# Performance work log

Hardware: AMD Instinct MI355X
Metric: run time of the kernel (lower is better)

## Reference

```python
import jax, jax.numpy as jnp
import numpy as np

BN_EPS = 1e-3          # nn.BatchNorm1d(..., eps=0.001)
NUM_PILLARS = 600000   # M = total occupied pillars across the batch
N_POINTS = 3_000_000
C_IN, C_OUT = 10, 64


def setup_inputs() -> dict:
    key = jax.random.key(0)
    k1, k2, k3 = jax.random.split(key, 3)
    pts_feature = jax.random.normal(k1, (N_POINTS, C_IN), dtype=jnp.float32)
    point_pillar_indices = jax.random.randint(k2, (N_POINTS,), 0, NUM_PILLARS, dtype=jnp.int32)
    # Linear(C_IN, C_OUT, bias=False), kaiming_normal init
    W = jax.random.normal(k3, (C_IN, C_OUT), dtype=jnp.float32) * np.sqrt(2.0 / C_IN)
    # BatchNorm1d in eval mode (running stats)
    gamma = jnp.ones((C_OUT,), jnp.float32)
    beta = jnp.zeros((C_OUT,), jnp.float32)
    run_mean = jnp.zeros((C_OUT,), jnp.float32)
    run_var = jnp.ones((C_OUT,), jnp.float32)
    return {"pts_feature": pts_feature, "point_pillar_indices": point_pillar_indices,
            "W": W, "gamma": gamma, "beta": beta, "run_mean": run_mean, "run_var": run_var}


def reference(pts_feature, point_pillar_indices, W, gamma, beta, run_mean, run_var):
    # shared MLP: Linear(no bias) -> BatchNorm1d(eval) -> ReLU, fused per-point
    h = pts_feature @ W                                        # (N, C_OUT)
    h = gamma * (h - run_mean) * jax.lax.rsqrt(run_var + BN_EPS) + beta
    h = jax.nn.relu(h)
    # scatter_max over irregular pillar ids -> (M, C_OUT)
    pooled = jax.ops.segment_max(h, point_pillar_indices, num_segments=NUM_PILLARS)
    # torch scatter_max leaves empty pillars at 0; jax gives -inf -> replace
    return jnp.where(jnp.isfinite(pooled), pooled, 0.0)
```

## Files before the change

### kernel.cpp

```cpp
#include <hip/hip_runtime.h>
#include <hip/hip_bf16.h>

#define C_IN 10
#define C_OUT 64
#define BN_EPS 1e-3f

#define BP    128
#define CB    256
#define NBMAX 4704
#define TS    2048

typedef __attribute__((ext_vector_type(8))) short bf16x8;
typedef __attribute__((ext_vector_type(4))) float f32x4;


__global__ __launch_bounds__(256) void k1_hist(const int* __restrict__ idx, int n, int chunk,
                                               unsigned* __restrict__ ghist, int NB) {
    __shared__ unsigned h[NBMAX];
    const int b = blockIdx.x, t = threadIdx.x;
    for (int i = t; i < NB; i += 256) h[i] = 0u;
    __syncthreads();
    const int lo = b * chunk;
    const int hi = min(n, lo + chunk);
    for (int i = lo + t; i < hi; i += 256)
        atomicAdd(&h[((unsigned)idx[i]) >> 7], 1u);
    __syncthreads();
    for (int k = t; k < NB; k += 256) ghist[(size_t)k * CB + b] = h[k];
}

__global__ __launch_bounds__(256) void k2a_reduce(const unsigned* __restrict__ g, int G,
                                                  unsigned* __restrict__ tsum) {
    __shared__ unsigned s[256];
    const int t = threadIdx.x;
    const int base = blockIdx.x * TS + t * 8;
    unsigned acc = 0;
#pragma unroll
    for (int j = 0; j < 8; ++j) { int gi = base + j; if (gi < G) acc += g[gi]; }
    s[t] = acc; __syncthreads();
    for (int off = 128; off > 0; off >>= 1) { if (t < off) s[t] += s[t + off]; __syncthreads(); }
    if (t == 0) tsum[blockIdx.x] = s[0];
}

__global__ __launch_bounds__(256) void k2b_scan(unsigned* __restrict__ tsum, int nt) {
    __shared__ unsigned partial[256], basev[256];
    const int t = threadIdx.x;
    const int per = (nt + 255) / 256;
    const int lo = t * per, hi = min(nt, lo + per);
    unsigned s = 0;
    for (int i = lo; i < hi; ++i) s += tsum[i];
    partial[t] = s; __syncthreads();
    if (t == 0) { unsigned a = 0; for (int k = 0; k < 256; ++k) { basev[k] = a; a += partial[k]; } }
    __syncthreads();
    unsigned a = basev[t];
    for (int i = lo; i < hi; ++i) { unsigned v = tsum[i]; tsum[i] = a; a += v; }
}

__global__ __launch_bounds__(256) void k2c_apply(unsigned* __restrict__ g, int G,
                                                 const unsigned* __restrict__ tsum,
                                                 unsigned* __restrict__ bstart, int NB, int n) {
    __shared__ unsigned s[256];
    const int t = threadIdx.x;
    const int base = blockIdx.x * TS + t * 8;
    unsigned v[8]; unsigned acc = 0;
#pragma unroll
    for (int j = 0; j < 8; ++j) { int gi = base + j; v[j] = (gi < G) ? g[gi] : 0u; acc += v[j]; }
    s[t] = acc; __syncthreads();
    for (int off = 1; off < 256; off <<= 1) {
        unsigned x = (t >= off) ? s[t - off] : 0u; __syncthreads();
        s[t] += x; __syncthreads();
    }
    unsigned excl = ((t == 0) ? 0u : s[t - 1]) + tsum[blockIdx.x];
#pragma unroll
    for (int j = 0; j < 8; ++j) {
        int gi = base + j;
        if (gi < G) {
            g[gi] = excl;
            if ((gi & (CB - 1)) == 0) bstart[gi / CB] = excl;
            excl += v[j];
        }
    }
    if (blockIdx.x == 0 && t == 0) bstart[NB] = (unsigned)n;
}

__global__ __launch_bounds__(256) void k3_scatter(const int* __restrict__ idx, int n, int chunk,
                                                  const unsigned* __restrict__ scanned,
                                                  unsigned* __restrict__ rec, int NB) {
    __shared__ unsigned cnt[NBMAX];
    __shared__ unsigned basel[NBMAX];
    const int b = blockIdx.x, t = threadIdx.x;
    for (int k = t; k < NB; k += 256) { basel[k] = scanned[(size_t)k * CB + b]; cnt[k] = 0u; }
    __syncthreads();
    const int lo = b * chunk, hi = min(n, lo + chunk);
    for (int i = lo + t; i < hi; i += 256) {
        unsigned pid = (unsigned)idx[i];
        unsigned k = pid >> 7;
        unsigned r = atomicAdd(&cnt[k], 1u);
        rec[basel[k] + r] = ((pid & 127u) << 22) | (unsigned)i;
    }
}


static __device__ __forceinline__ unsigned pk2(float2 v) {
    __hip_bfloat162 h = __float22bfloat162_rn(v);
    return *reinterpret_cast<unsigned*>(&h);
}

__global__ __launch_bounds__(256) void pool_mfma2_kernel(
    const float* __restrict__ pts,
    const unsigned* __restrict__ rec,
    const unsigned* __restrict__ bstart,
    const float* __restrict__ W,
    const float* __restrict__ gamma, const float* __restrict__ beta,
    const float* __restrict__ mean, const float* __restrict__ var,
    float* __restrict__ out, int M)
{
    __shared__ unsigned smax[BP * C_OUT];

    const int b = blockIdx.x, t = threadIdx.x;
    const int lane = t & 63, w = t >> 6;
    const int g = lane >> 4, c0 = lane & 15;

    uint4* s4 = (uint4*)smax;
    const uint4 zq = make_uint4(0u, 0u, 0u, 0u);
    for (int i = t; i < BP * C_OUT / 4; i += 256) s4[i] = zq;

    bf16x8 bfrag[4];
#pragma unroll
    for (int tc = 0; tc < 4; ++tc) {
        const int ch = 16 * tc + c0;
        const float sc = gamma[ch] * rsqrtf(var[ch] + BN_EPS);
        const float sh = fmaf(-mean[ch], sc, beta[ch]);
        union { bf16x8 v; unsigned short u[8]; } B;
#pragma unroll
        for (int j = 0; j < 8; ++j) {
            const int k = g * 8 + j;
            float val = 0.f;
            if (k < 10) val = W[k * C_OUT + ch] * sc;
            else if (k == 10) val = sh;
            __hip_bfloat16 hb = __float2bfloat16(val);
            B.u[j] = *reinterpret_cast<unsigned short*>(&hb);
        }
        bfrag[tc] = B.v;
    }

    const unsigned base = bstart[b];
    const int T = (int)(bstart[b + 1] - base);

    __syncthreads();

    float2 pf0, pf1, pf2, pf3, pf4;
    unsigned rc = 0u;
    if (w * 64 < T) {
        const int i = min(w * 64 + lane, T - 1);
        rc = rec[base + i];
        const float2* f2 = (const float2*)(pts + (size_t)(rc & 0x3FFFFFu) * C_IN);
        pf0 = f2[0]; pf1 = f2[1]; pf2 = f2[2]; pf3 = f2[3]; pf4 = f2[4];
    }

    for (int k = 0; w * 64 + k * 256 < T; ++k) {
        const unsigned p0 = pk2(pf0), p1 = pk2(pf1), p2 = pk2(pf2),
                       p3 = pk2(pf3), p4 = pk2(pf4);
        const int lpv = (int)(rc >> 22);

        const int nb_ = w * 64 + (k + 1) * 256;
        if (nb_ < T) {
            const int i = min(nb_ + lane, T - 1);
            rc = rec[base + i];
            const float2* f2 = (const float2*)(pts + (size_t)(rc & 0x3FFFFFu) * C_IN);
            pf0 = f2[0]; pf1 = f2[1]; pf2 = f2[2]; pf3 = f2[3]; pf4 = f2[4];
        }

#pragma unroll
        for (int ti = 0; ti < 4; ++ti) {
            const int srcA = ti * 16 + c0;
            const unsigned s0 = (unsigned)__shfl((int)p0, srcA);
            const unsigned s1 = (unsigned)__shfl((int)p1, srcA);
            const unsigned s2 = (unsigned)__shfl((int)p2, srcA);
            const unsigned s3 = (unsigned)__shfl((int)p3, srcA);
            const unsigned s4v = (unsigned)__shfl((int)p4, srcA);
            union { uint4 q; bf16x8 v; } A;
            if (g == 0)      A.q = make_uint4(s0, s1, s2, s3);
            else if (g == 1) A.q = make_uint4(s4v, 0x00003F80u, 0u, 0u);
            else             A.q = make_uint4(0u, 0u, 0u, 0u);

            const f32x4 z4 = {0.f, 0.f, 0.f, 0.f};
            f32x4 a0 = __builtin_amdgcn_mfma_f32_16x16x32_bf16(A.v, bfrag[0], z4, 0, 0, 0);
            f32x4 a1 = __builtin_amdgcn_mfma_f32_16x16x32_bf16(A.v, bfrag[1], z4, 0, 0, 0);
            f32x4 a2 = __builtin_amdgcn_mfma_f32_16x16x32_bf16(A.v, bfrag[2], z4, 0, 0, 0);
            f32x4 a3 = __builtin_amdgcn_mfma_f32_16x16x32_bf16(A.v, bfrag[3], z4, 0, 0, 0);

            const int sb = ti * 16 + g * 4;
            const int l0 = __shfl(lpv, sb + 0);
            const int l1 = __shfl(lpv, sb + 1);
            const int l2 = __shfl(lpv, sb + 2);
            const int l3 = __shfl(lpv, sb + 3);

#define CONSUME_R(LP, R) { \
            unsigned* rowp = &smax[((unsigned)(LP)) << 6]; \
            const unsigned rb = (unsigned)(c0 + ((LP) << 2)); \
            atomicMax(&rowp[(rb +  0u) & 63u], __float_as_uint(fmaxf(a0[R], 0.f))); \
            atomicMax(&rowp[(rb + 16u) & 63u], __float_as_uint(fmaxf(a1[R], 0.f))); \
            atomicMax(&rowp[(rb + 32u) & 63u], __float_as_uint(fmaxf(a2[R], 0.f))); \
            atomicMax(&rowp[(rb + 48u) & 63u], __float_as_uint(fmaxf(a3[R], 0.f))); }
            CONSUME_R(l0, 0); CONSUME_R(l1, 1); CONSUME_R(l2, 2); CONSUME_R(l3, 3);
#undef CONSUME_R
        }
    }
    __syncthreads();

    const int row = t >> 1;
    const int half = t & 1;
    const int gp = b * BP + row;
    if (gp < M) {
        float4* o4 = (float4*)out;
        const size_t ob = (size_t)gp * (C_OUT / 4);
#pragma unroll
        for (int j = 0; j < 8; ++j) {
            const int q = half * 8 + j;
            uint4 v = s4[row * 16 + q];
            const int oq = (q - row) & 15;
            o4[ob + oq] = *reinterpret_cast<float4*>(&v);
        }
    }
}

#define CHUNK 256
#define FSTRIDE 11

__global__ __launch_bounds__(256) void zero_u32_kernel(unsigned* __restrict__ p, int n) {
    int i = blockIdx.x * 256 + threadIdx.x;
    int s = gridDim.x * 256;
    for (; i < n; i += s) p[i] = 0u;
}

__global__ __launch_bounds__(256) void hist_kernel(const int* __restrict__ idx, int n,
                                                   unsigned* __restrict__ hist, int nb) {
    __shared__ unsigned h[NBMAX];
    for (int i = threadIdx.x; i < nb; i += 256) h[i] = 0u;
    __syncthreads();
    int stride = gridDim.x * 256;
    for (int i = blockIdx.x * 256 + threadIdx.x; i < n; i += stride)
        atomicAdd(&h[((unsigned)idx[i]) >> 7], 1u);
    __syncthreads();
    for (int i = threadIdx.x; i < nb; i += 256) {
        unsigned v = h[i];
        if (v) atomicAdd(&hist[i], v);
    }
}

__global__ __launch_bounds__(256) void scan_kernel(const unsigned* __restrict__ hist,
                                                   unsigned* __restrict__ cursor, int nb) {
    __shared__ unsigned partial[256];
    __shared__ unsigned base[256];
    int per = (nb + 255) / 256;
    int lo = threadIdx.x * per;
    int hi = lo + per; if (hi > nb) hi = nb;
    unsigned s = 0;
    for (int i = lo; i < hi; ++i) s += hist[i];
    partial[threadIdx.x] = s;
    __syncthreads();
    if (threadIdx.x == 0) {
        unsigned acc = 0;
        for (int t = 0; t < 256; ++t) { base[t] = acc; acc += partial[t]; }
    }
    __syncthreads();
    unsigned acc = base[threadIdx.x];
    for (int i = lo; i < hi; ++i) { cursor[i] = acc; acc += hist[i]; }
}

__global__ __launch_bounds__(256) void scatter_ids_kernel(const int* __restrict__ idx, int n,
                                                          unsigned* __restrict__ cursor,
                                                          unsigned* __restrict__ rec) {
    int stride = gridDim.x * 256;
    for (int i = blockIdx.x * 256 + threadIdx.x; i < n; i += stride) {
        unsigned pid = (unsigned)idx[i];
        unsigned pos = atomicAdd(&cursor[pid >> 7], 1u);
        rec[pos] = ((pid & (BP - 1)) << 22) | (unsigned)i;
    }
}

__global__ __launch_bounds__(256) void pool_kernel(
    const float* __restrict__ pts, const unsigned* __restrict__ rec,
    const unsigned* __restrict__ cursor, const float* __restrict__ W,
    const float* __restrict__ gamma, const float* __restrict__ beta,
    const float* __restrict__ mean, const float* __restrict__ var,
    float* __restrict__ out, int M)
{
    __shared__ unsigned smax[BP * C_OUT];
    __shared__ float    feat[CHUNK * FSTRIDE];
    __shared__ unsigned slp[CHUNK];
    const int b = blockIdx.x, t = threadIdx.x;
    const int lane = t & 63, wid = t >> 6;
    for (int i = t; i < BP * C_OUT; i += 256) smax[i] = 0u;
    float w[C_IN];
#pragma unroll
    for (int j = 0; j < C_IN; ++j) w[j] = W[j * C_OUT + lane];
    const float scale = gamma[lane] * rsqrtf(var[lane] + BN_EPS);
    const float shift = fmaf(-mean[lane], scale, beta[lane]);
    const unsigned start = (b == 0) ? 0u : cursor[b - 1];
    const int total = (int)(cursor[b] - start);
    float fr[C_IN]; unsigned rcr = 0; bool hav = false;
    if (t < total) {
        rcr = rec[start + t];
        const float2* f2 = (const float2*)(pts + (size_t)(rcr & 0x3FFFFFu) * C_IN);
#pragma unroll
        for (int j = 0; j < 5; ++j) { float2 v = f2[j]; fr[2*j] = v.x; fr[2*j+1] = v.y; }
        hav = true;
    }
    for (int chunk = 0; chunk < total; chunk += CHUNK) {
        const int nrec = min(CHUNK, total - chunk);
        __syncthreads();
        if (hav) {
            slp[t] = rcr >> 22;
#pragma unroll
            for (int j = 0; j < C_IN; ++j) feat[t * FSTRIDE + j] = fr[j];
        }
        __syncthreads();
        const int nr = chunk + CHUNK + t;
        hav = false;
        if (nr < total) {
            rcr = rec[start + nr];
            const float2* f2 = (const float2*)(pts + (size_t)(rcr & 0x3FFFFFu) * C_IN);
#pragma unroll
            for (int j = 0; j < 5; ++j) { float2 v = f2[j]; fr[2*j] = v.x; fr[2*j+1] = v.y; }
            hav = true;
        }
        for (int i = wid; i < nrec; i += 4) {
            const unsigned lp = slp[i];
            const float* f = &feat[i * FSTRIDE];
            float h = 0.f;
#pragma unroll
            for (int j = 0; j < C_IN; ++j) h = fmaf(f[j], w[j], h);
            h = fmaxf(fmaf(h, scale, shift), 0.f);
            atomicMax(&smax[(lp << 6) + lane], __float_as_uint(h));
        }
    }
    __syncthreads();
    const float4* sf4 = (const float4*)smax;
    float4* o4 = (float4*)out;
    const size_t base4 = (size_t)b * (BP * C_OUT / 4);
    const size_t tot4  = (size_t)M * (C_OUT / 4);
    for (int i = t; i < BP * C_OUT / 4; i += 256) {
        size_t gq = base4 + (size_t)i;
        if (gq < tot4) o4[gq] = sf4[i];
    }
}

__global__ __launch_bounds__(256) void zero_out_kernel(float4* __restrict__ out4, int n4) {
    int i = blockIdx.x * blockDim.x + threadIdx.x;
    int stride = gridDim.x * blockDim.x;
    float4 z = make_float4(0.f, 0.f, 0.f, 0.f);
    for (int j = i; j < n4; j += stride) out4[j] = z;
}

__global__ __launch_bounds__(256) void pillar_scatter_kernel(
    const float* __restrict__ pts, const int* __restrict__ idx,
    const float* __restrict__ W, const float* __restrict__ gamma,
    const float* __restrict__ beta, const float* __restrict__ mean,
    const float* __restrict__ var, unsigned int* __restrict__ out, int npoints)
{
    const int lane = threadIdx.x & 63;
    float w[C_IN];
#pragma unroll
    for (int j = 0; j < C_IN; ++j) w[j] = W[j * C_OUT + lane];
    const float scale = gamma[lane] * rsqrtf(var[lane] + BN_EPS);
    const float shift = fmaf(-mean[lane], scale, beta[lane]);
    const int wave_id = (blockIdx.x * blockDim.x + threadIdx.x) >> 6;
    const int nwaves  = (gridDim.x * blockDim.x) >> 6;
    for (int p = wave_id; p < npoints; p += nwaves) {
        const float* f = pts + (size_t)p * C_IN;
        float h = 0.f;
#pragma unroll
        for (int j = 0; j < C_IN; ++j) h = fmaf(f[j], w[j], h);
        h = fmaxf(fmaf(h, scale, shift), 0.f);
        atomicMax(&out[(size_t)idx[p] * C_OUT + lane], __float_as_uint(h));
    }
}


extern "C" void kernel_launch(void* const* d_in, const int* in_sizes, int n_in,
                              void* d_out, int out_size, void* d_ws, size_t ws_size,
                              hipStream_t stream) {
    const float* pts   = (const float*)d_in[0];
    const int*   idx   = (const int*)  d_in[1];
    const float* W     = (const float*)d_in[2];
    const float* gamma = (const float*)d_in[3];
    const float* beta  = (const float*)d_in[4];
    const float* mean  = (const float*)d_in[5];
    const float* var   = (const float*)d_in[6];

    const int npoints = in_sizes[0] / C_IN;
    const int M       = out_size / C_OUT;
    const int NB      = (M + BP - 1) / BP;
    const int G       = NB * CB;
    const int nt      = (G + TS - 1) / TS;
    const int chunk   = (npoints + CB - 1) / CB;

    const size_t rec_off = (((size_t)G + (size_t)nt + (size_t)NB + 1) + 63) & ~(size_t)63;
    const size_t need    = (rec_off + (size_t)npoints) * sizeof(unsigned);

    if (NB <= NBMAX && npoints < (1 << 22) && nt <= 65535 && ws_size >= need) {
        unsigned* ghist  = (unsigned*)d_ws;
        unsigned* tsum   = ghist + G;
        unsigned* bstart = tsum + nt;
        unsigned* rec    = (unsigned*)d_ws + rec_off;

        k1_hist           <<<CB, 256, 0, stream>>>(idx, npoints, chunk, ghist, NB);
        k2a_reduce        <<<nt, 256, 0, stream>>>(ghist, G, tsum);
        k2b_scan          <<<1,  256, 0, stream>>>(tsum, nt);
        k2c_apply         <<<nt, 256, 0, stream>>>(ghist, G, tsum, bstart, NB, npoints);
        k3_scatter        <<<CB, 256, 0, stream>>>(idx, npoints, chunk, ghist, rec, NB);
        pool_mfma2_kernel <<<NB, 256, 0, stream>>>(pts, rec, bstart, W, gamma, beta,
                                                   mean, var, (float*)d_out, M);
        return;
    }

    const size_t rec_off_f1 = ((size_t)(2 * NB) + 63) & ~(size_t)63;
    const size_t need_f1    = (rec_off_f1 + (size_t)npoints) * sizeof(unsigned);
    if (NB <= NBMAX && npoints < (1 << 22) && ws_size >= need_f1) {
        unsigned* cursor = (unsigned*)d_ws;
        unsigned* hist   = cursor + NB;
        unsigned* rec    = (unsigned*)d_ws + rec_off_f1;
        zero_u32_kernel<<<(2 * NB + 255) / 256, 256, 0, stream>>>(cursor, 2 * NB);
        hist_kernel<<<256, 256, 0, stream>>>(idx, npoints, hist, NB);
        scan_kernel<<<1, 256, 0, stream>>>(hist, cursor, NB);
        scatter_ids_kernel<<<2048, 256, 0, stream>>>(idx, npoints, cursor, rec);
        pool_kernel<<<NB, 256, 0, stream>>>(pts, rec, cursor, W, gamma, beta, mean, var,
                                            (float*)d_out, M);
        return;
    }

    zero_out_kernel<<<2048, 256, 0, stream>>>((float4*)d_out, out_size / 4);
    pillar_scatter_kernel<<<2048, 256, 0, stream>>>(
        pts, idx, W, gamma, beta, mean, var, (unsigned int*)d_out, npoints);
}
```

Baseline: 210.8 us.

## Scatter packed bf16 features into sorted records and pool with 512 threads

The scatter pass now reads each point's features sequentially and writes a 24-byte record: five packed bf16 pairs plus the local pillar id, in bucket order. The pool kernel then streams these contiguous records instead of gathering 40-byte rows from random point indices. This trades a random gather in the pool stage for extra writes in the scatter and a larger workspace. The pool kernel also uses 512 threads, a different bank-rotation for the shared atomics, and per-row coalesced output writes. The old fallback path is removed, and the previous index-only path is kept for when the workspace is too small.

New measurement: 266.4 us. 26.4% more time.

```diff
diff --git a/kernel.cpp b/kernel.cpp
--- a/kernel.cpp
+++ b/kernel.cpp
@@ -12,6 +12,7 @@
 
 typedef __attribute__((ext_vector_type(8))) short bf16x8;
 typedef __attribute__((ext_vector_type(4))) float f32x4;
+typedef unsigned long long u64;
 
 
 __global__ __launch_bounds__(256) void k1_hist(const int* __restrict__ idx, int n, int chunk,
@@ -82,9 +83,15 @@
     if (blockIdx.x == 0 && t == 0) bstart[NB] = (unsigned)n;
 }
 
-__global__ __launch_bounds__(256) void k3_scatter(const int* __restrict__ idx, int n, int chunk,
-                                                  const unsigned* __restrict__ scanned,
-                                                  unsigned* __restrict__ rec, int NB) {
+static __device__ __forceinline__ unsigned pk2(float2 v) {
+    __hip_bfloat162 h = __float22bfloat162_rn(v);
+    return *reinterpret_cast<unsigned*>(&h);
+}
+
+__global__ __launch_bounds__(256) void k3b_scatter_feats(
+    const int* __restrict__ idx, const float* __restrict__ pts, int n, int chunk,
+    const unsigned* __restrict__ scanned, u64* __restrict__ rec2, int NB)
+{
     __shared__ unsigned cnt[NBMAX];
     __shared__ unsigned basel[NBMAX];
     const int b = blockIdx.x, t = threadIdx.x;
@@ -92,22 +99,20 @@
     __syncthreads();
     const int lo = b * chunk, hi = min(n, lo + chunk);
     for (int i = lo + t; i < hi; i += 256) {
-        unsigned pid = (unsigned)idx[i];
-        unsigned k = pid >> 7;
-        unsigned r = atomicAdd(&cnt[k], 1u);
-        rec[basel[k] + r] = ((pid & 127u) << 22) | (unsigned)i;
-    }
-}
-
-
-static __device__ __forceinline__ unsigned pk2(float2 v) {
-    __hip_bfloat162 h = __float22bfloat162_rn(v);
-    return *reinterpret_cast<unsigned*>(&h);
-}
-
-__global__ __launch_bounds__(256) void pool_mfma2_kernel(
-    const float* __restrict__ pts,
-    const unsigned* __restrict__ rec,
+        const unsigned pid = (unsigned)idx[i];
+        const float2* f2 = (const float2*)(pts + (size_t)i * C_IN);
+        const float2 a0 = f2[0], a1 = f2[1], a2 = f2[2], a3 = f2[3], a4 = f2[4];
+        const unsigned k = pid >> 7;
+        const unsigned r = atomicAdd(&cnt[k], 1u);
+        u64* o = rec2 + (size_t)(basel[k] + r) * 3;
+        o[0] = (u64)pk2(a0) | ((u64)pk2(a1) << 32);
+        o[1] = (u64)pk2(a2) | ((u64)pk2(a3) << 32);
+        o[2] = (u64)pk2(a4) | ((u64)(pid & 127u) << 32);
+    }
+}
+
+__global__ __launch_bounds__(512) void pool_rec_kernel(
+    const u64* __restrict__ rec2,
     const unsigned* __restrict__ bstart,
     const float* __restrict__ W,
     const float* __restrict__ gamma, const float* __restrict__ beta,
@@ -122,7 +127,7 @@
 
     uint4* s4 = (uint4*)smax;
     const uint4 zq = make_uint4(0u, 0u, 0u, 0u);
-    for (int i = t; i < BP * C_OUT / 4; i += 256) s4[i] = zq;
+    for (int i = t; i < BP * C_OUT / 4; i += 512) s4[i] = zq;
 
     bf16x8 bfrag[4];
 #pragma unroll
@@ -148,26 +153,24 @@
 
     __syncthreads();
 
-    float2 pf0, pf1, pf2, pf3, pf4;
-    unsigned rc = 0u;
+    u64 q0 = 0, q1 = 0, q2 = 0;
     if (w * 64 < T) {
         const int i = min(w * 64 + lane, T - 1);
-        rc = rec[base + i];
-        const float2* f2 = (const float2*)(pts + (size_t)(rc & 0x3FFFFFu) * C_IN);
-        pf0 = f2[0]; pf1 = f2[1]; pf2 = f2[2]; pf3 = f2[3]; pf4 = f2[4];
-    }
-
-    for (int k = 0; w * 64 + k * 256 < T; ++k) {
-        const unsigned p0 = pk2(pf0), p1 = pk2(pf1), p2 = pk2(pf2),
-                       p3 = pk2(pf3), p4 = pk2(pf4);
-        const int lpv = (int)(rc >> 22);
-
-        const int nb_ = w * 64 + (k + 1) * 256;
+        const u64* r = rec2 + (size_t)(base + i) * 3;
+        q0 = r[0]; q1 = r[1]; q2 = r[2];
+    }
+
+    for (int k = 0; w * 64 + k * 512 < T; ++k) {
+        const unsigned p0 = (unsigned)q0, p1 = (unsigned)(q0 >> 32);
+        const unsigned p2 = (unsigned)q1, p3 = (unsigned)(q1 >> 32);
+        const unsigned p4 = (unsigned)q2;
+        const int lpv = (int)(unsigned)(q2 >> 32);
+
+        const int nb_ = w * 64 + (k + 1) * 512;
         if (nb_ < T) {
             const int i = min(nb_ + lane, T - 1);
-            rc = rec[base + i];
-            const float2* f2 = (const float2*)(pts + (size_t)(rc & 0x3FFFFFu) * C_IN);
-            pf0 = f2[0]; pf1 = f2[1]; pf2 = f2[2]; pf3 = f2[3]; pf4 = f2[4];
+            const u64* r = rec2 + (size_t)(base + i) * 3;
+            q0 = r[0]; q1 = r[1]; q2 = r[2];
         }
 
 #pragma unroll
@@ -197,7 +200,7 @@
 
 #define CONSUME_R(LP, R) { \
             unsigned* rowp = &smax[((unsigned)(LP)) << 6]; \
-            const unsigned rb = (unsigned)(c0 + ((LP) << 2)); \
+            const unsigned rb = (unsigned)(c0 + (LP)); \
             atomicMax(&rowp[(rb +  0u) & 63u], __float_as_uint(fmaxf(a0[R], 0.f))); \
             atomicMax(&rowp[(rb + 16u) & 63u], __float_as_uint(fmaxf(a1[R], 0.f))); \
             atomicMax(&rowp[(rb + 32u) & 63u], __float_as_uint(fmaxf(a2[R], 0.f))); \
@@ -208,141 +211,128 @@
     }
     __syncthreads();
 
-    const int row = t >> 1;
-    const int half = t & 1;
-    const int gp = b * BP + row;
-    if (gp < M) {
-        float4* o4 = (float4*)out;
-        const size_t ob = (size_t)gp * (C_OUT / 4);
-#pragma unroll
-        for (int j = 0; j < 8; ++j) {
-            const int q = half * 8 + j;
-            uint4 v = s4[row * 16 + q];
-            const int oq = (q - row) & 15;
-            o4[ob + oq] = *reinterpret_cast<float4*>(&v);
-        }
-    }
-}
-
-#define CHUNK 256
-#define FSTRIDE 11
-
-__global__ __launch_bounds__(256) void zero_u32_kernel(unsigned* __restrict__ p, int n) {
-    int i = blockIdx.x * 256 + threadIdx.x;
-    int s = gridDim.x * 256;
-    for (; i < n; i += s) p[i] = 0u;
-}
-
-__global__ __launch_bounds__(256) void hist_kernel(const int* __restrict__ idx, int n,
-                                                   unsigned* __restrict__ hist, int nb) {
-    __shared__ unsigned h[NBMAX];
-    for (int i = threadIdx.x; i < nb; i += 256) h[i] = 0u;
-    __syncthreads();
-    int stride = gridDim.x * 256;
-    for (int i = blockIdx.x * 256 + threadIdx.x; i < n; i += stride)
-        atomicAdd(&h[((unsigned)idx[i]) >> 7], 1u);
-    __syncthreads();
-    for (int i = threadIdx.x; i < nb; i += 256) {
-        unsigned v = h[i];
-        if (v) atomicAdd(&hist[i], v);
-    }
-}
-
-__global__ __launch_bounds__(256) void scan_kernel(const unsigned* __restrict__ hist,
-                                                   unsigned* __restrict__ cursor, int nb) {
-    __shared__ unsigned partial[256];
-    __shared__ unsigned base[256];
-    int per = (nb + 255) / 256;
-    int lo = threadIdx.x * per;
-    int hi = lo + per; if (hi > nb) hi = nb;
-    unsigned s = 0;
-    for (int i = lo; i < hi; ++i) s += hist[i];
-    partial[threadIdx.x] = s;
-    __syncthreads();
-    if (threadIdx.x == 0) {
-        unsigned acc = 0;
-        for (int t = 0; t < 256; ++t) { base[t] = acc; acc += partial[t]; }
-    }
-    __syncthreads();
-    unsigned acc = base[threadIdx.x];
-    for (int i = lo; i < hi; ++i) { cursor[i] = acc; acc += hist[i]; }
-}
-
-__global__ __launch_bounds__(256) void scatter_ids_kernel(const int* __restrict__ idx, int n,
-                                                          unsigned* __restrict__ cursor,
-                                                          unsigned* __restrict__ rec) {
-    int stride = gridDim.x * 256;
-    for (int i = blockIdx.x * 256 + threadIdx.x; i < n; i += stride) {
+    for (int row = w; row < BP; row += 8) {
+        const int gp = b * BP + row;
+        if (gp < M) {
+            const unsigned v = smax[row * 64 + ((lane + row) & 63)];
+            out[(size_t)gp * C_OUT + lane] = __uint_as_float(v);
+        }
+    }
+}
+
+__global__ __launch_bounds__(256) void k3_scatter(const int* __restrict__ idx, int n, int chunk,
+                                                  const unsigned* __restrict__ scanned,
+                                                  unsigned* __restrict__ rec, int NB) {
+    __shared__ unsigned cnt[NBMAX];
+    __shared__ unsigned basel[NBMAX];
+    const int b = blockIdx.x, t = threadIdx.x;
+    for (int k = t; k < NB; k += 256) { basel[k] = scanned[(size_t)k * CB + b]; cnt[k] = 0u; }
+    __syncthreads();
+    const int lo = b * chunk, hi = min(n, lo + chunk);
+    for (int i = lo + t; i < hi; i += 256) {
         unsigned pid = (unsigned)idx[i];
-        unsigned pos = atomicAdd(&cursor[pid >> 7], 1u);
-        rec[pos] = ((pid & (BP - 1)) << 22) | (unsigned)i;
-    }
-}
-
-__global__ __launch_bounds__(256) void pool_kernel(
-    const float* __restrict__ pts, const unsigned* __restrict__ rec,
-    const unsigned* __restrict__ cursor, const float* __restrict__ W,
+        unsigned k = pid >> 7;
+        unsigned r = atomicAdd(&cnt[k], 1u);
+        rec[basel[k] + r] = ((pid & 127u) << 22) | (unsigned)i;
+    }
+}
+
+__global__ __launch_bounds__(256) void pool_mfma2_kernel(
+    const float* __restrict__ pts,
+    const unsigned* __restrict__ rec,
+    const unsigned* __restrict__ bstart,
+    const float* __restrict__ W,
     const float* __restrict__ gamma, const float* __restrict__ beta,
     const float* __restrict__ mean, const float* __restrict__ var,
     float* __restrict__ out, int M)
 {
     __shared__ unsigned smax[BP * C_OUT];
-    __shared__ float    feat[CHUNK * FSTRIDE];
-    __shared__ unsigned slp[CHUNK];
     const int b = blockIdx.x, t = threadIdx.x;
-    const int lane = t & 63, wid = t >> 6;
-    for (int i = t; i < BP * C_OUT; i += 256) smax[i] = 0u;
-    float w[C_IN];
-#pragma unroll
-    for (int j = 0; j < C_IN; ++j) w[j] = W[j * C_OUT + lane];
-    const float scale = gamma[lane] * rsqrtf(var[lane] + BN_EPS);
-    const float shift = fmaf(-mean[lane], scale, beta[lane]);
-    const unsigned start = (b == 0) ? 0u : cursor[b - 1];
-    const int total = (int)(cursor[b] - start);
-    float fr[C_IN]; unsigned rcr = 0; bool hav = false;
-    if (t < total) {
-        rcr = rec[start + t];
-        const float2* f2 = (const float2*)(pts + (size_t)(rcr & 0x3FFFFFu) * C_IN);
-#pragma unroll
-        for (int j = 0; j < 5; ++j) { float2 v = f2[j]; fr[2*j] = v.x; fr[2*j+1] = v.y; }
-        hav = true;
-    }
-    for (int chunk = 0; chunk < total; chunk += CHUNK) {
-        const int nrec = min(CHUNK, total - chunk);
-        __syncthreads();
-        if (hav) {
-            slp[t] = rcr >> 22;
-#pragma unroll
-            for (int j = 0; j < C_IN; ++j) feat[t * FSTRIDE + j] = fr[j];
-        }
-        __syncthreads();
-        const int nr = chunk + CHUNK + t;
-        hav = false;
-        if (nr < total) {
-            rcr = rec[start + nr];
-            const float2* f2 = (const float2*)(pts + (size_t)(rcr & 0x3FFFFFu) * C_IN);
-#pragma unroll
-            for (int j = 0; j < 5; ++j) { float2 v = f2[j]; fr[2*j] = v.x; fr[2*j+1] = v.y; }
-            hav = true;
-        }
-        for (int i = wid; i < nrec; i += 4) {
-            const unsigned lp = slp[i];
-            const float* f = &feat[i * FSTRIDE];
-            float h = 0.f;
-#pragma unroll
-            for (int j = 0; j < C_IN; ++j) h = fmaf(f[j], w[j], h);
-            h = fmaxf(fmaf(h, scale, shift), 0.f);
-            atomicMax(&smax[(lp << 6) + lane], __float_as_uint(h));
-        }
-    }
-    __syncthreads();
-    const float4* sf4 = (const float4*)smax;
-    float4* o4 = (float4*)out;
-    const size_t base4 = (size_t)b * (BP * C_OUT / 4);
-    const size_t tot4  = (size_t)M * (C_OUT / 4);
-    for (int i = t; i < BP * C_OUT / 4; i += 256) {
-        size_t gq = base4 + (size_t)i;
-        if (gq < tot4) o4[gq] = sf4[i];
+    const int lane = t & 63, w = t >> 6;
+    const int g = lane >> 4, c0 = lane & 15;
+    uint4* s4 = (uint4*)smax;
+    const uint4 zq = make_uint4(0u, 0u, 0u, 0u);
+    for (int i = t; i < BP * C_OUT / 4; i += 256) s4[i] = zq;
+    bf16x8 bfrag[4];
+#pragma unroll
+    for (int tc = 0; tc < 4; ++tc) {
+        const int ch = 16 * tc + c0;
+        const float sc = gamma[ch] * rsqrtf(var[ch] + BN_EPS);
+        const float sh = fmaf(-mean[ch], sc, beta[ch]);
+        union { bf16x8 v; unsigned short u[8]; } B;
+#pragma unroll
+        for (int j = 0; j < 8; ++j) {
+            const int k = g * 8 + j;
+            float val = 0.f;
+            if (k < 10) val = W[k * C_OUT + ch] * sc;
+            else if (k == 10) val = sh;
+            __hip_bfloat16 hb = __float2bfloat16(val);
+            B.u[j] = *reinterpret_cast<unsigned short*>(&hb);
+        }
+        bfrag[tc] = B.v;
+    }
+    const unsigned base = bstart[b];
+    const int T = (int)(bstart[b + 1] - base);
+    __syncthreads();
+    float2 pf0, pf1, pf2, pf3, pf4;
+    unsigned rc = 0u;
+    if (w * 64 < T) {
+        const int i = min(w * 64 + lane, T - 1);
+        rc = rec[base + i];
+        const float2* f2 = (const float2*)(pts + (size_t)(rc & 0x3FFFFFu) * C_IN);
+        pf0 = f2[0]; pf1 = f2[1]; pf2 = f2[2]; pf3 = f2[3]; pf4 = f2[4];
+    }
+    for (int k = 0; w * 64 + k * 256 < T; ++k) {
+        const unsigned p0 = pk2(pf0), p1 = pk2(pf1), p2 = pk2(pf2),
+                       p3 = pk2(pf3), p4 = pk2(pf4);
+        const int lpv = (int)(rc >> 22);
+        const int nb_ = w * 64 + (k + 1) * 256;
+        if (nb_ < T) {
+            const int i = min(nb_ + lane, T - 1);
+            rc = rec[base + i];
+            const float2* f2 = (const float2*)(pts + (size_t)(rc & 0x3FFFFFu) * C_IN);
+            pf0 = f2[0]; pf1 = f2[1]; pf2 = f2[2]; pf3 = f2[3]; pf4 = f2[4];
+        }
+#pragma unroll
+        for (int ti = 0; ti < 4; ++ti) {
+            const int srcA = ti * 16 + c0;
+            const unsigned s0 = (unsigned)__shfl((int)p0, srcA);
+            const unsigned s1 = (unsigned)__shfl((int)p1, srcA);
+            const unsigned s2 = (unsigned)__shfl((int)p2, srcA);
+            const unsigned s3 = (unsigned)__shfl((int)p3, srcA);
+            const unsigned s4v = (unsigned)__shfl((int)p4, srcA);
+            union { uint4 q; bf16x8 v; } A;
+            if (g == 0)      A.q = make_uint4(s0, s1, s2, s3);
+            else if (g == 1) A.q = make_uint4(s4v, 0x00003F80u, 0u, 0u);
+            else             A.q = make_uint4(0u, 0u, 0u, 0u);
+            const f32x4 z4 = {0.f, 0.f, 0.f, 0.f};
+            f32x4 a0 = __builtin_amdgcn_mfma_f32_16x16x32_bf16(A.v, bfrag[0], z4, 0, 0, 0);
+            f32x4 a1 = __builtin_amdgcn_mfma_f32_16x16x32_bf16(A.v, bfrag[1], z4, 0, 0, 0);
+            f32x4 a2 = __builtin_amdgcn_mfma_f32_16x16x32_bf16(A.v, bfrag[2], z4, 0, 0, 0);
+            f32x4 a3 = __builtin_amdgcn_mfma_f32_16x16x32_bf16(A.v, bfrag[3], z4, 0, 0, 0);
+            const int sb = ti * 16 + g * 4;
+            const int l0 = __shfl(lpv, sb + 0);
+            const int l1 = __shfl(lpv, sb + 1);
+            const int l2 = __shfl(lpv, sb + 2);
+            const int l3 = __shfl(lpv, sb + 3);
+#define CONSUME_R(LP, R) { \
+            unsigned* rowp = &smax[((unsigned)(LP)) << 6]; \
+            const unsigned rb = (unsigned)(c0 + (LP)); \
+            atomicMax(&rowp[(rb +  0u) & 63u], __float_as_uint(fmaxf(a0[R], 0.f))); \
+            atomicMax(&rowp[(rb + 16u) & 63u], __float_as_uint(fmaxf(a1[R], 0.f))); \
+            atomicMax(&rowp[(rb + 32u) & 63u], __float_as_uint(fmaxf(a2[R], 0.f))); \
+            atomicMax(&rowp[(rb + 48u) & 63u], __float_as_uint(fmaxf(a3[R], 0.f))); }
+            CONSUME_R(l0, 0); CONSUME_R(l1, 1); CONSUME_R(l2, 2); CONSUME_R(l3, 3);
+#undef CONSUME_R
+        }
+    }
+    __syncthreads();
+    for (int row = w; row < BP; row += 4) {
+        const int gp = b * BP + row;
+        if (gp < M) {
+            const unsigned v = smax[row * 64 + ((lane + row) & 63)];
+            out[(size_t)gp * C_OUT + lane] = __uint_as_float(v);
+        }
     }
 }
 
@@ -396,14 +386,34 @@
     const int nt      = (G + TS - 1) / TS;
     const int chunk   = (npoints + CB - 1) / CB;
 
-    const size_t rec_off = (((size_t)G + (size_t)nt + (size_t)NB + 1) + 63) & ~(size_t)63;
-    const size_t need    = (rec_off + (size_t)npoints) * sizeof(unsigned);
-
-    if (NB <= NBMAX && npoints < (1 << 22) && nt <= 65535 && ws_size >= need) {
+    const size_t head_u32  = (size_t)G + (size_t)nt + (size_t)NB + 1;
+    const size_t head_b    = ((head_u32 * 4) + 63) & ~(size_t)63;
+    const size_t need_rec2 = head_b + (size_t)npoints * 24;
+    const size_t need_rec1 = head_b + (size_t)npoints * 4;
+
+    const bool shape_ok = (NB <= NBMAX) && (npoints < (1 << 22)) && (nt <= 65535);
+
+    if (shape_ok && ws_size >= need_rec2) {
         unsigned* ghist  = (unsigned*)d_ws;
         unsigned* tsum   = ghist + G;
         unsigned* bstart = tsum + nt;
-        unsigned* rec    = (unsigned*)d_ws + rec_off;
+        u64*      rec2   = (u64*)((char*)d_ws + head_b);
+
+        k1_hist          <<<CB, 256, 0, stream>>>(idx, npoints, chunk, ghist, NB);
+        k2a_reduce       <<<nt, 256, 0, stream>>>(ghist, G, tsum);
+        k2b_scan         <<<1,  256, 0, stream>>>(tsum, nt);
+        k2c_apply        <<<nt, 256, 0, stream>>>(ghist, G, tsum, bstart, NB, npoints);
+        k3b_scatter_feats<<<CB, 256, 0, stream>>>(idx, pts, npoints, chunk, ghist, rec2, NB);
+        pool_rec_kernel  <<<NB, 512, 0, stream>>>(rec2, bstart, W, gamma, beta,
+                                                  mean, var, (float*)d_out, M);
+        return;
+    }
+
+    if (shape_ok && ws_size >= need_rec1) {
+        unsigned* ghist  = (unsigned*)d_ws;
+        unsigned* tsum   = ghist + G;
+        unsigned* bstart = tsum + nt;
+        unsigned* rec    = (unsigned*)((char*)d_ws + head_b);
 
         k1_hist           <<<CB, 256, 0, stream>>>(idx, npoints, chunk, ghist, NB);
         k2a_reduce        <<<nt, 256, 0, stream>>>(ghist, G, tsum);
@@ -415,21 +425,6 @@
         return;
     }
 
-    const size_t rec_off_f1 = ((size_t)(2 * NB) + 63) & ~(size_t)63;
-    const size_t need_f1    = (rec_off_f1 + (size_t)npoints) * sizeof(unsigned);
-    if (NB <= NBMAX && npoints < (1 << 22) && ws_size >= need_f1) {
-        unsigned* cursor = (unsigned*)d_ws;
-        unsigned* hist   = cursor + NB;
-        unsigned* rec    = (unsigned*)d_ws + rec_off_f1;
-        zero_u32_kernel<<<(2 * NB + 255) / 256, 256, 0, stream>>>(cursor, 2 * NB);
-        hist_kernel<<<256, 256, 0, stream>>>(idx, npoints, hist, NB);
-        scan_kernel<<<1, 256, 0, stream>>>(hist, cursor, NB);
-        scatter_ids_kernel<<<2048, 256, 0, stream>>>(idx, npoints, cursor, rec);
-        pool_kernel<<<NB, 256, 0, stream>>>(pts, rec, cursor, W, gamma, beta, mean, var,
-                                            (float*)d_out, M);
-        return;
-    }
-
     zero_out_kernel<<<2048, 256, 0, stream>>>((float4*)d_out, out_size / 4);
     pillar_scatter_kernel<<<2048, 256, 0, stream>>>(
         pts, idx, W, gamma, beta, mean, var, (unsigned int*)d_out, npoints);
```
